# Kernel tuning notes

Measured on AMD Instinct MI355X. Metric: run time of the kernel, lower is better.

Reference implementation:

```python
import jax, jax.numpy as jnp
import numpy as np

N_NODES = 10000
N_EDGES = 160000
HID = 256
NBOND = 6
NATOM = 62
NLAYERS = 6


def _lin_init(key, fan_in, fan_out):
    # torch nn.Linear default: U(-1/sqrt(fan_in), 1/sqrt(fan_in))
    kw, kb = jax.random.split(key)
    bound = 1.0 / np.sqrt(fan_in)
    w = jax.random.uniform(kw, (fan_in, fan_out), jnp.float32, -bound, bound)
    b = jax.random.uniform(kb, (fan_out,), jnp.float32, -bound, bound)
    return w, b


def setup_inputs() -> dict:
    key = jax.random.key(0)
    ks = jax.random.split(key, 32)
    atom_features = jax.random.normal(ks[0], (N_NODES, NATOM), jnp.float32)
    edge_index = jax.random.randint(ks[1], (2, N_EDGES), 0, N_NODES, jnp.int64 if jax.config.jax_enable_x64 else jnp.int32)
    edge_features = jax.random.normal(ks[2], (N_EDGES, NBOND), jnp.float32)

    embed_w, embed_b = _lin_init(ks[3], NATOM, HID)

    msg_in = 2 * HID + NBOND  # 518
    mw1, mb1, mw2, mb2 = [], [], [], []
    uw1, ub1, uw2, ub2 = [], [], [], []
    for i in range(NLAYERS):
        k = jax.random.split(ks[4 + i], 4)
        w, b = _lin_init(k[0], msg_in, HID); mw1.append(w); mb1.append(b)
        w, b = _lin_init(k[1], HID, HID); mw2.append(w); mb2.append(b)
        w, b = _lin_init(k[2], 2 * HID, HID); uw1.append(w); ub1.append(b)
        w, b = _lin_init(k[3], HID, HID); uw2.append(w); ub2.append(b)

    r_w1, r_b1 = _lin_init(ks[20], HID, HID)
    r_w2, r_b2 = _lin_init(ks[21], HID, HID // 2)
    r_w3, r_b3 = _lin_init(ks[22], HID // 2, 1)

    return {
        "atom_features": atom_features,
        "edge_index": edge_index,
        "edge_features": edge_features,
        "embed_w": embed_w, "embed_b": embed_b,
        "msg_w1": jnp.stack(mw1), "msg_b1": jnp.stack(mb1),
        "msg_w2": jnp.stack(mw2), "msg_b2": jnp.stack(mb2),
        "upd_w1": jnp.stack(uw1), "upd_b1": jnp.stack(ub1),
        "upd_w2": jnp.stack(uw2), "upd_b2": jnp.stack(ub2),
        "r_w1": r_w1, "r_b1": r_b1,
        "r_w2": r_w2, "r_b2": r_b2,
        "r_w3": r_w3, "r_b3": r_b3,
    }


def _mlp2(x, w1, b1, w2, b2):
    return jnp.maximum(x @ w1 + b1, 0.0) @ w2 + b2


def reference(atom_features, edge_index, edge_features,
              embed_w, embed_b,
              msg_w1, msg_b1, msg_w2, msg_b2,
              upd_w1, upd_b1, upd_w2, upd_b2,
              r_w1, r_b1, r_w2, r_b2, r_w3, r_b3):
    src, dst = edge_index[0], edge_index[1]
    n = atom_features.shape[0]
    x = atom_features @ embed_w + embed_b  # [N, H]
    for l in range(msg_w1.shape[0]):
        # per-edge gather + concat -> message MLP
        msg_in = jnp.concatenate([x[src], x[dst], edge_features], axis=-1)  # [E, 2H+B]
        msgs = _mlp2(msg_in, msg_w1[l], msg_b1[l], msg_w2[l], msg_b2[l])  # [E, H]
        # scatter-add into dst nodes
        agg = jax.ops.segment_sum(msgs, dst, num_segments=n)  # [N, H]
        x = _mlp2(jnp.concatenate([x, agg], axis=-1), upd_w1[l], upd_b1[l], upd_w2[l], upd_b2[l])
    # readout (dropout is identity in eval mode)
    h = jnp.maximum(x @ r_w1 + r_b1, 0.0)
    h = jnp.maximum(h @ r_w2 + r_b2, 0.0)
    out = h @ r_w3 + r_b3  # [N, 1]
    return out.mean(axis=0)  # [1]
```

## Files before the change

kernel.cpp:

```cpp
#include <hip/hip_runtime.h>
#include <hip/hip_bf16.h>
#include <hip/hip_fp16.h>


#define HID 256

typedef _Float16 h8 __attribute__((ext_vector_type(8)));
typedef float f32x4 __attribute__((ext_vector_type(4)));

__device__ __forceinline__ void unpack_h8(const int4& r, float* f) {
    const __half2* h = reinterpret_cast<const __half2*>(&r);
#pragma unroll
    for (int k = 0; k < 4; ++k) {
        float2 t = __half22float2(h[k]);
        f[2 * k] = t.x;
        f[2 * k + 1] = t.y;
    }
}

__device__ __forceinline__ void unpack_h4(const int2& r, float* f) {
    const __half2* h = reinterpret_cast<const __half2*>(&r);
    float2 t0 = __half22float2(h[0]);
    float2 t1 = __half22float2(h[1]);
    f[0] = t0.x; f[1] = t0.y; f[2] = t1.x; f[3] = t1.y;
}

__device__ __forceinline__ void gld16(const void* g, void* l) {
    __builtin_amdgcn_global_load_lds(
        (const __attribute__((address_space(1))) void*)g,
        (__attribute__((address_space(3))) void*)l, 16, 0, 0);
}

__device__ __forceinline__ int swz(int row) { return (row + (row >> 2)) & 3; }


struct CDesc {
    const float* src;
    __half* dst;
    int Kreal, Kpad, srcN, tile0, dstStride;
};
struct CTab {
    CDesc d[32];
    int nd;
};

__device__ void convert_body(const CTab& tab, int bid) {
    int idx = 0;
    for (int i = 1; i < tab.nd; ++i)
        if (tab.d[i].tile0 <= bid) idx = i;
    const CDesc d = tab.d[idx];
    const int q = bid - d.tile0;
    const int ntN = d.srcN >> 6;
    const int kb = (q / ntN) * 32;
    const int nb = (q % ntN) * 64;
    const int n = nb + (threadIdx.x & 63);
    const int k0 = kb + (threadIdx.x >> 6) * 8;
    h8 v;
#pragma unroll
    for (int j = 0; j < 8; ++j) {
        int k = k0 + j;
        v[j] = (_Float16)((k < d.Kreal) ? d.src[(size_t)k * d.srcN + n] : 0.f);
    }
    *reinterpret_cast<h8*>(&d.dst[(size_t)n * d.dstStride + k0]) = v;
}


__global__ void hist_conv_kernel(const int* __restrict__ dst, int* __restrict__ deg,
                                 int E, const float* __restrict__ atom,
                                 __half* __restrict__ atomH, int NA,
                                 int histB, CTab tab) {
    if ((int)blockIdx.x < histB) {
        int i = blockIdx.x * blockDim.x + threadIdx.x;
        if (i < E) atomicAdd(&deg[dst[i]], 1);
        if (i < NA) {
            int r = i >> 3, seg = i & 7;
            h8 v;
#pragma unroll
            for (int j = 0; j < 8; ++j) {
                int c = seg * 8 + j;
                v[j] = (_Float16)((c < 62) ? atom[(size_t)r * 62 + c] : 0.f);
            }
            *reinterpret_cast<h8*>(&atomH[(size_t)r * 64 + seg * 8]) = v;
        }
    } else {
        convert_body(tab, blockIdx.x - histB);
    }
}

__global__ __launch_bounds__(256) void scan_kernel(
    const int* __restrict__ deg, int* __restrict__ offs, float* __restrict__ degf, int n) {
    __shared__ int ws[4];
    const int t = threadIdx.x;
    const int lane = t & 63;
    const int w = t >> 6;
    const int per = (n + 255) / 256;
    const int s = t * per;
    const int e = min(s + per, n);
    int sum = 0;
    for (int i = s; i < e; ++i) sum += deg[i];
    int v = sum;
#pragma unroll
    for (int off = 1; off < 64; off <<= 1) {
        int u = __shfl_up(v, off, 64);
        if (lane >= off) v += u;
    }
    if (lane == 63) ws[w] = v;
    __syncthreads();
    if (t == 0) {
        int c = 0;
#pragma unroll
        for (int i = 0; i < 4; ++i) { int x = ws[i]; ws[i] = c; c += x; }
    }
    __syncthreads();
    int run = ws[w] + v - sum;
    for (int i = s; i < e; ++i) {
        int d = deg[i];
        offs[i] = run;
        degf[i] = (float)d;
        run += d;
    }
    if (e == n) offs[n] = run;
}


struct BDesc { float* out; const float* base; const float* v1; const float* B1;
               const float* v2; const float* B2; };
struct BTab { BDesc d[31]; };


#define ASTR 40

struct FDesc { const float* U2; const __half* Wfb; __half* dst; int stride; };
struct FTab { FDesc d[22]; };

__device__ void fold_tile(unsigned char* ldsraw, const FDesc& dd, int t4) {
    _Float16* Ah = (_Float16*)ldsraw;
    _Float16* Bh = (_Float16*)(ldsraw + 64 * ASTR * 2);
    const int rowBase = (t4 >> 2) * 64;
    const int colBase = (t4 & 3) * 64;

    const int tid = threadIdx.x;
    const int lane = tid & 63;
    const int wave = tid >> 6;
    const int waveM = (wave >> 1) * 32;
    const int waveN = (wave & 1) * 32;
    const int m0 = lane & 15;
    const int quad = lane >> 4;
    const int sr = tid >> 2;
    const int sseg = tid & 3;

    const f32x4 z = {0.f, 0.f, 0.f, 0.f};
    f32x4 acc[2][2] = {{z, z}, {z, z}};

    for (int kb = 0; kb < 256; kb += 32) {
        {
            size_t off = (size_t)(rowBase + sr) * 256 + kb + sseg * 8;
            *reinterpret_cast<int4*>(&Ah[sr * ASTR + sseg * 8]) =
                *reinterpret_cast<const int4*>(&dd.Wfb[off]);
        }
        {
            const float* Bp = dd.U2 + (size_t)(colBase + sr) * 256 + kb + sseg * 8;
            float4 u0 = *reinterpret_cast<const float4*>(Bp);
            float4 u1 = *reinterpret_cast<const float4*>(Bp + 4);
            h8 v;
            v[0] = (_Float16)u0.x; v[1] = (_Float16)u0.y;
            v[2] = (_Float16)u0.z; v[3] = (_Float16)u0.w;
            v[4] = (_Float16)u1.x; v[5] = (_Float16)u1.y;
            v[6] = (_Float16)u1.z; v[7] = (_Float16)u1.w;
            *reinterpret_cast<h8*>(&Bh[sr * ASTR + sseg * 8]) = v;
        }
        __syncthreads();

        const h8 a0 = *reinterpret_cast<const h8*>(&Ah[(waveM + m0) * ASTR + quad * 8]);
        const h8 a1 = *reinterpret_cast<const h8*>(&Ah[(waveM + 16 + m0) * ASTR + quad * 8]);
        const h8 b0 = *reinterpret_cast<const h8*>(&Bh[(waveN + m0) * ASTR + quad * 8]);
        const h8 b1 = *reinterpret_cast<const h8*>(&Bh[(waveN + 16 + m0) * ASTR + quad * 8]);

        acc[0][0] = __builtin_amdgcn_mfma_f32_16x16x32_f16(a0, b0, acc[0][0], 0, 0, 0);
        acc[0][1] = __builtin_amdgcn_mfma_f32_16x16x32_f16(a0, b1, acc[0][1], 0, 0, 0);
        acc[1][0] = __builtin_amdgcn_mfma_f32_16x16x32_f16(a1, b0, acc[1][0], 0, 0, 0);
        acc[1][1] = __builtin_amdgcn_mfma_f32_16x16x32_f16(a1, b1, acc[1][1], 0, 0, 0);

        __syncthreads();
    }

#pragma unroll
    for (int tm = 0; tm < 2; ++tm)
#pragma unroll
        for (int reg = 0; reg < 4; ++reg) {
            int n = rowBase + waveM + tm * 16 + quad * 4 + reg;
#pragma unroll
            for (int tn = 0; tn < 2; ++tn) {
                int k = colBase + waveN + tn * 16 + m0;
                dd.dst[(size_t)n * dd.stride + k] = __float2half_rn(acc[tm][tn][reg]);
            }
        }
}


template <int TN>
__device__ void gemm_tile(
    unsigned char* lds, int bx, int by,
    const __half* __restrict__ A, int lda,
    const __half* __restrict__ W, int K,
    const float* __restrict__ bias,
    __half* __restrict__ C, int M, int Nc, int do_relu) {
    constexpr int BUF = 4096 + TN * 2048;

    const int tid = threadIdx.x;
    const int lane = tid & 63;
    const int wave = tid >> 6;
    const int m0 = lane & 15;
    const int quad = lane >> 4;
    const int waveM = (wave >> 1) * 32;
    const int waveN = (wave & 1) * (TN * 16);
    const int rowBase = bx * 64;
    const int colBase = by * (TN * 32);

    const int sa_r = tid >> 2;
    const int sa_ks = (tid & 3) ^ swz(sa_r);
    const int sa_row = min(rowBase + sa_r, M - 1);
    const int sb_r1 = sa_r + 64;
    const int sb_ks1 = (tid & 3) ^ swz(sb_r1);

    int aoff[2], boff[TN];
#pragma unroll
    for (int tm = 0; tm < 2; ++tm) {
        int r = waveM + tm * 16 + m0;
        aoff[tm] = ((r << 2) + (quad ^ swz(r))) << 4;
    }
#pragma unroll
    for (int tn = 0; tn < TN; ++tn) {
        int r = waveN + tn * 16 + m0;
        boff[tn] = 4096 + (((r << 2) + (quad ^ swz(r))) << 4);
    }

    const f32x4 z = {0.f, 0.f, 0.f, 0.f};
    f32x4 acc[2][TN];
#pragma unroll
    for (int tm = 0; tm < 2; ++tm)
#pragma unroll
        for (int tn = 0; tn < TN; ++tn) acc[tm][tn] = z;

    const __half* ga = A + (size_t)sa_row * lda + sa_ks * 8;
    const __half* gb0 = W + (size_t)(colBase + sa_r) * K + sa_ks * 8;
    const __half* gb1 = W + (size_t)(colBase + sb_r1) * K + sb_ks1 * 8;

    auto issue = [&](int p, int kb) {
        unsigned char* base = lds + p * BUF;
        gld16(ga + kb, base + wave * 1024);
        gld16(gb0 + kb, base + 4096 + wave * 1024);
        if constexpr (TN == 4) gld16(gb1 + kb, base + 8192 + wave * 1024);
    };

    issue(0, 0);
    int p = 0;
    for (int kb = 0; kb < K; kb += 32) {
        const bool has_next = (kb + 32 < K);
        if (has_next) issue(p ^ 1, kb + 32);
        if (has_next) {
            if constexpr (TN == 4)
                asm volatile("s_waitcnt vmcnt(3)" ::: "memory");
            else
                asm volatile("s_waitcnt vmcnt(2)" ::: "memory");
        } else {
            asm volatile("s_waitcnt vmcnt(0)" ::: "memory");
        }
        asm volatile("s_barrier" ::: "memory");

        const unsigned char* base = lds + p * BUF;
        h8 ah[2], bh[TN];
#pragma unroll
        for (int tm = 0; tm < 2; ++tm)
            ah[tm] = *reinterpret_cast<const h8*>(base + aoff[tm]);
#pragma unroll
        for (int tn = 0; tn < TN; ++tn)
            bh[tn] = *reinterpret_cast<const h8*>(base + boff[tn]);
#pragma unroll
        for (int tm = 0; tm < 2; ++tm)
#pragma unroll
            for (int tn = 0; tn < TN; ++tn)
                acc[tm][tn] = __builtin_amdgcn_mfma_f32_16x16x32_f16(
                    ah[tm], bh[tn], acc[tm][tn], 0, 0, 0);
        asm volatile("s_waitcnt lgkmcnt(0)" ::: "memory");
        asm volatile("s_barrier" ::: "memory");
        p ^= 1;
    }

    float cb[TN];
    int col[TN];
#pragma unroll
    for (int tn = 0; tn < TN; ++tn) {
        col[tn] = colBase + waveN + tn * 16 + m0;
        cb[tn] = bias ? bias[col[tn]] : 0.f;
    }
#pragma unroll
    for (int tm = 0; tm < 2; ++tm) {
#pragma unroll
        for (int reg = 0; reg < 4; ++reg) {
            int row = rowBase + waveM + tm * 16 + quad * 4 + reg;
            if (row >= M) continue;
#pragma unroll
            for (int tn = 0; tn < TN; ++tn) {
                float v = acc[tm][tn][reg] + cb[tn];
                if (do_relu) v = fmaxf(v, 0.f);
                C[(size_t)row * Nc + col[tn]] = __float2half_rn(v);
            }
        }
    }
}


__global__ __launch_bounds__(256) void scatter_fold_bias_embed_kernel(
    const int* __restrict__ src, const int* __restrict__ dst,
    const int* __restrict__ offs, int* __restrict__ cursor,
    int* __restrict__ csr_src, const float* __restrict__ ef,
    __half* __restrict__ ef8, int E, int sblocks,
    FTab ft, BTab bt, int fblocks, int bblocks,
    const __half* __restrict__ atomH, const __half* __restrict__ w_emb,
    const float* __restrict__ emb_b, __half* __restrict__ outX,
    int M, int mblk64) {
    __shared__ __align__(16) unsigned char lds[16384];
    int b = blockIdx.x;
    if (b < sblocks) {
        int i = b * 256 + (int)threadIdx.x;
        if (i < E) {
            int d = dst[i];
            int pos = atomicAdd(&cursor[d], 1);
            int idx = offs[d] + pos;
            csr_src[idx] = src[i];
            const float* s6 = ef + (size_t)i * 6;
            unsigned short h[8];
#pragma unroll
            for (int j = 0; j < 6; ++j) h[j] = __half_as_ushort(__float2half_rn(s6[j]));
            h[6] = 0; h[7] = 0;
            int4 pk;
            pk.x = (int)(h[0] | ((unsigned)h[1] << 16));
            pk.y = (int)(h[2] | ((unsigned)h[3] << 16));
            pk.z = (int)(h[4] | ((unsigned)h[5] << 16));
            pk.w = (int)(h[6] | ((unsigned)h[7] << 16));
            *reinterpret_cast<int4*>(ef8 + (size_t)idx * 8) = pk;
        }
        return;
    }
    b -= sblocks;
    if (b < fblocks) {
        fold_tile(lds, ft.d[b >> 4], b & 15);
        return;
    }
    b -= fblocks;
    if (b < bblocks) {
        const BDesc d = bt.d[b];
        const int j = threadIdx.x;
        float acc = d.base ? d.base[j] : 0.f;
        if (d.v1)
            for (int k = 0; k < 256; ++k) acc = fmaf(d.v1[k], d.B1[(size_t)k * 256 + j], acc);
        if (d.v2)
            for (int k = 0; k < 256; ++k) acc = fmaf(d.v2[k], d.B2[(size_t)k * 256 + j], acc);
        d.out[j] = acc;
        return;
    }
    b -= bblocks;
    gemm_tile<2>(lds, b % mblk64, b / mblk64, atomH, 64, w_emb, 64,
                 emb_b, outX, M, HID, 0);
}


__global__ __launch_bounds__(256) void gemm128(
    const __half* __restrict__ A, int lda, const __half* __restrict__ A2,
    const __half* __restrict__ W, int K,
    const float* __restrict__ bias, const float* __restrict__ bias2,
    const float* __restrict__ rowscale,
    __half* __restrict__ C, int M, int Nc, int do_relu) {
    __shared__ __align__(16) unsigned char lds[2 * 16384];

    const int tid = threadIdx.x;
    const int lane = tid & 63;
    const int wave = tid >> 6;
    const int m0 = lane & 15;
    const int quad = lane >> 4;
    const int waveM = (wave >> 1) * 64;
    const int waveN = (wave & 1) * 64;
    const int rowBase = (int)blockIdx.x * 128;
    const int colBase = (int)blockIdx.y * 128;

    const __half* ga[2];
    const __half* ga2[2];
    const __half* gb[2];
    int adst[2], bdst[2];
#pragma unroll
    for (int j = 0; j < 2; ++j) {
        int seg = j * 256 + wave * 64 + lane;
        int r = seg >> 2;
        int ks = (seg & 3) ^ swz(r);
        int arow = min(rowBase + r, M - 1);
        ga[j] = A + (size_t)arow * lda + ks * 8;
        ga2[j] = A2 ? A2 + (size_t)arow * lda + ks * 8 : nullptr;
        gb[j] = W + (size_t)(colBase + r) * K + ks * 8;
        adst[j] = (j * 4 + wave) * 1024;
        bdst[j] = 8192 + (j * 4 + wave) * 1024;
    }

    int aoff[4], boff[4];
#pragma unroll
    for (int i = 0; i < 4; ++i) {
        int r = waveM + i * 16 + m0;
        aoff[i] = ((r << 2) + (quad ^ swz(r))) << 4;
        int rb = waveN + i * 16 + m0;
        boff[i] = 8192 + (((rb << 2) + (quad ^ swz(rb))) << 4);
    }

    const f32x4 z = {0.f, 0.f, 0.f, 0.f};
    f32x4 acc[4][4];
#pragma unroll
    for (int i = 0; i < 4; ++i)
#pragma unroll
        for (int j = 0; j < 4; ++j) acc[i][j] = z;

    auto issue = [&](int p, int kb) {
        unsigned char* base = lds + p * 16384;
        const bool hi = (A2 != nullptr) && (kb >= 256);
        const int ko = hi ? (kb - 256) : kb;
#pragma unroll
        for (int j = 0; j < 2; ++j)
            gld16((hi ? ga2[j] : ga[j]) + ko, base + adst[j]);
#pragma unroll
        for (int j = 0; j < 2; ++j)
            gld16(gb[j] + kb, base + bdst[j]);
    };

    issue(0, 0);
    int p = 0;
    for (int kb = 0; kb < K; kb += 32) {
        const bool has_next = (kb + 32 < K);
        if (has_next) issue(p ^ 1, kb + 32);
        if (has_next) asm volatile("s_waitcnt vmcnt(4)" ::: "memory");
        else          asm volatile("s_waitcnt vmcnt(0)" ::: "memory");
        asm volatile("s_barrier" ::: "memory");

        const unsigned char* base = lds + p * 16384;
        h8 ah[4], bh[4];
#pragma unroll
        for (int i = 0; i < 4; ++i) ah[i] = *reinterpret_cast<const h8*>(base + aoff[i]);
#pragma unroll
        for (int j = 0; j < 4; ++j) bh[j] = *reinterpret_cast<const h8*>(base + boff[j]);
#pragma unroll
        for (int i = 0; i < 4; ++i)
#pragma unroll
            for (int j = 0; j < 4; ++j)
                acc[i][j] = __builtin_amdgcn_mfma_f32_16x16x32_f16(
                    ah[i], bh[j], acc[i][j], 0, 0, 0);
        asm volatile("s_waitcnt lgkmcnt(0)" ::: "memory");
        asm volatile("s_barrier" ::: "memory");
        p ^= 1;
    }

    float cb[4], db[4];
    int col[4];
#pragma unroll
    for (int j = 0; j < 4; ++j) {
        col[j] = colBase + waveN + j * 16 + m0;
        cb[j] = bias ? bias[col[j]] : 0.f;
        db[j] = bias2 ? bias2[col[j]] : 0.f;
    }
#pragma unroll
    for (int i = 0; i < 4; ++i) {
#pragma unroll
        for (int reg = 0; reg < 4; ++reg) {
            int row = rowBase + waveM + i * 16 + quad * 4 + reg;
            if (row >= M) continue;
            float rs = rowscale ? rowscale[row] : 0.0f;
#pragma unroll
            for (int j = 0; j < 4; ++j) {
                float v = acc[i][j][reg] + cb[j] + rs * db[j];
                if (do_relu) v = fmaxf(v, 0.f);
                C[(size_t)row * Nc + col[j]] = __float2half_rn(v);
            }
        }
    }
}


__global__ __launch_bounds__(256) void aggregate_kernel(
    const __half* __restrict__ PQ, const __half* __restrict__ ef8,
    const int* __restrict__ offs, const int* __restrict__ csr_src,
    const float* __restrict__ W1c, __half* __restrict__ Hagg, int n) {
    const int wave = threadIdx.x >> 6;
    const int lane = threadIdx.x & 63;
    const int node = blockIdx.x * 4 + wave;
    if (node >= n) return;
    const int ch = lane * 4;

    float wc[6][4];
#pragma unroll
    for (int k = 0; k < 6; ++k) {
        float4 w0 = *reinterpret_cast<const float4*>(W1c + k * HID + ch);
        wc[k][0] = w0.x; wc[k][1] = w0.y; wc[k][2] = w0.z; wc[k][3] = w0.w;
    }
    float qb[4];
    unpack_h4(*reinterpret_cast<const int2*>(PQ + (size_t)node * 512 + 256 + ch), qb);

    float acc[4] = {0.f, 0.f, 0.f, 0.f};

    auto fma_edge = [&](const int2& praw, const int4& eraw) {
        float p[4], e[8];
        unpack_h4(praw, p);
        unpack_h8(eraw, e);
#pragma unroll
        for (int i = 0; i < 4; ++i) {
            float h = p[i] + qb[i];
            h = fmaf(e[0], wc[0][i], h);
            h = fmaf(e[1], wc[1][i], h);
            h = fmaf(e[2], wc[2][i], h);
            h = fmaf(e[3], wc[3][i], h);
            h = fmaf(e[4], wc[4][i], h);
            h = fmaf(e[5], wc[5][i], h);
            acc[i] += fmaxf(h, 0.f);
        }
    };

    const int beg = offs[node];
    const int end = offs[node + 1];
    int j = beg;

    while (j + 6 <= end) {
        int s0 = csr_src[j];
        int s1 = csr_src[j + 1];
        int s2 = csr_src[j + 2];
        int s3 = csr_src[j + 3];
        int s4 = csr_src[j + 4];
        int s5 = csr_src[j + 5];
        int4 e0 = *reinterpret_cast<const int4*>(ef8 + (size_t)j * 8);
        int4 e1 = *reinterpret_cast<const int4*>(ef8 + (size_t)(j + 1) * 8);
        int4 e2 = *reinterpret_cast<const int4*>(ef8 + (size_t)(j + 2) * 8);
        int4 e3 = *reinterpret_cast<const int4*>(ef8 + (size_t)(j + 3) * 8);
        int4 e4 = *reinterpret_cast<const int4*>(ef8 + (size_t)(j + 4) * 8);
        int4 e5 = *reinterpret_cast<const int4*>(ef8 + (size_t)(j + 5) * 8);
        int2 p0 = *reinterpret_cast<const int2*>(PQ + (size_t)s0 * 512 + ch);
        int2 p1 = *reinterpret_cast<const int2*>(PQ + (size_t)s1 * 512 + ch);
        int2 p2 = *reinterpret_cast<const int2*>(PQ + (size_t)s2 * 512 + ch);
        int2 p3 = *reinterpret_cast<const int2*>(PQ + (size_t)s3 * 512 + ch);
        int2 p4 = *reinterpret_cast<const int2*>(PQ + (size_t)s4 * 512 + ch);
        int2 p5 = *reinterpret_cast<const int2*>(PQ + (size_t)s5 * 512 + ch);
        fma_edge(p0, e0);
        fma_edge(p1, e1);
        fma_edge(p2, e2);
        fma_edge(p3, e3);
        fma_edge(p4, e4);
        fma_edge(p5, e5);
        j += 6;
    }
    while (j + 2 <= end) {
        int s0 = csr_src[j];
        int s1 = csr_src[j + 1];
        int4 e0 = *reinterpret_cast<const int4*>(ef8 + (size_t)j * 8);
        int4 e1 = *reinterpret_cast<const int4*>(ef8 + (size_t)(j + 1) * 8);
        int2 p0 = *reinterpret_cast<const int2*>(PQ + (size_t)s0 * 512 + ch);
        int2 p1 = *reinterpret_cast<const int2*>(PQ + (size_t)s1 * 512 + ch);
        fma_edge(p0, e0);
        fma_edge(p1, e1);
        j += 2;
    }
    if (j < end) {
        int s = csr_src[j];
        int4 e = *reinterpret_cast<const int4*>(ef8 + (size_t)j * 8);
        int2 pw = *reinterpret_cast<const int2*>(PQ + (size_t)s * 512 + ch);
        fma_edge(pw, e);
    }

    unsigned short hs[4];
#pragma unroll
    for (int i = 0; i < 4; ++i) hs[i] = __half_as_ushort(__float2half_rn(acc[i]));
    int2 pk;
    pk.x = (int)(hs[0] | ((unsigned)hs[1] << 16));
    pk.y = (int)(hs[2] | ((unsigned)hs[3] << 16));
    *reinterpret_cast<int2*>(Hagg + (size_t)node * HID + ch) = pk;
}


__global__ __launch_bounds__(256) void readout_kernel(
    const __half* __restrict__ U5, const __half* __restrict__ wF,
    const float* __restrict__ cbF, const __half* __restrict__ wR2,
    const float* __restrict__ bR2, const float* __restrict__ w3,
    const float* __restrict__ b3, float* __restrict__ accum,
    int* __restrict__ done, float* __restrict__ outp, int M, int nblocks) {
    __shared__ __align__(16) unsigned char lds[24576 + 64 * 272 * 2];
    _Float16* h1 = (_Float16*)(lds + 24576);

    const int tid = threadIdx.x;
    const int lane = tid & 63;
    const int wave = tid >> 6;
    const int m0 = lane & 15;
    const int quad = lane >> 4;
    const int waveM = (wave >> 1) * 32;
    const int waveN = (wave & 1) * 64;
    const int rowBase = blockIdx.x * 64;

    const int sa_r = tid >> 2;
    const int sa_ks = (tid & 3) ^ swz(sa_r);
    const int sa_row = min(rowBase + sa_r, M - 1);
    const int sb_r1 = sa_r + 64;
    const int sb_ks1 = (tid & 3) ^ swz(sb_r1);

    int aoff[2], boff[4];
#pragma unroll
    for (int tm = 0; tm < 2; ++tm) {
        int r = waveM + tm * 16 + m0;
        aoff[tm] = ((r << 2) + (quad ^ swz(r))) << 4;
    }
#pragma unroll
    for (int tn = 0; tn < 4; ++tn) {
        int r = waveN + tn * 16 + m0;
        boff[tn] = (((r << 2) + (quad ^ swz(r))) << 4);
    }

    constexpr int BUF = 4096 + 4 * 2048;
    const f32x4 z = {0.f, 0.f, 0.f, 0.f};

    for (int half = 0; half < 2; ++half) {
        const __half* W = wF + (size_t)(half * 128) * 256;
        f32x4 acc[2][4] = {{z, z, z, z}, {z, z, z, z}};
        const __half* ga = U5 + (size_t)sa_row * 256 + sa_ks * 8;
        const __half* gb0 = W + (size_t)sa_r * 256 + sa_ks * 8;
        const __half* gb1 = W + (size_t)sb_r1 * 256 + sb_ks1 * 8;

        auto issue = [&](int p, int kb) {
            unsigned char* base = lds + p * BUF;
            gld16(ga + kb, base + wave * 1024);
            gld16(gb0 + kb, base + 4096 + wave * 1024);
            gld16(gb1 + kb, base + 8192 + wave * 1024);
        };
        issue(0, 0);
        int p = 0;
        for (int kb = 0; kb < 256; kb += 32) {
            const bool has_next = (kb + 32 < 256);
            if (has_next) issue(p ^ 1, kb + 32);
            if (has_next) asm volatile("s_waitcnt vmcnt(3)" ::: "memory");
            else asm volatile("s_waitcnt vmcnt(0)" ::: "memory");
            asm volatile("s_barrier" ::: "memory");
            const unsigned char* base = lds + p * BUF;
            h8 ah[2], bh[4];
#pragma unroll
            for (int tm = 0; tm < 2; ++tm)
                ah[tm] = *reinterpret_cast<const h8*>(base + aoff[tm]);
#pragma unroll
            for (int tn = 0; tn < 4; ++tn)
                bh[tn] = *reinterpret_cast<const h8*>(base + 4096 + boff[tn]);
#pragma unroll
            for (int tm = 0; tm < 2; ++tm)
#pragma unroll
                for (int tn = 0; tn < 4; ++tn)
                    acc[tm][tn] = __builtin_amdgcn_mfma_f32_16x16x32_f16(
                        ah[tm], bh[tn], acc[tm][tn], 0, 0, 0);
            asm volatile("s_waitcnt lgkmcnt(0)" ::: "memory");
            asm volatile("s_barrier" ::: "memory");
            p ^= 1;
        }
#pragma unroll
        for (int tm = 0; tm < 2; ++tm)
#pragma unroll
            for (int reg = 0; reg < 4; ++reg) {
                int r = waveM + tm * 16 + quad * 4 + reg;
#pragma unroll
                for (int tn = 0; tn < 4; ++tn) {
                    int c = half * 128 + waveN + tn * 16 + m0;
                    float v = acc[tm][tn][reg] + cbF[c];
                    h1[r * 272 + c] = (_Float16)fmaxf(v, 0.f);
                }
            }
        __syncthreads();
    }

    f32x4 acc2[2][4] = {{z, z, z, z}, {z, z, z, z}};
    auto issueB = [&](int p, int kb) {
        unsigned char* base = lds + p * 8192;
        gld16(wR2 + (size_t)sa_r * 256 + sa_ks * 8 + kb, base + wave * 1024);
        gld16(wR2 + (size_t)sb_r1 * 256 + sb_ks1 * 8 + kb, base + 4096 + wave * 1024);
    };
    issueB(0, 0);
    int p = 0;
    for (int kb = 0; kb < 256; kb += 32) {
        const bool has_next = (kb + 32 < 256);
        if (has_next) issueB(p ^ 1, kb + 32);
        if (has_next) asm volatile("s_waitcnt vmcnt(2)" ::: "memory");
        else asm volatile("s_waitcnt vmcnt(0)" ::: "memory");
        asm volatile("s_barrier" ::: "memory");
        const unsigned char* base = lds + p * 8192;
        h8 ah[2], bh[4];
#pragma unroll
        for (int tm = 0; tm < 2; ++tm)
            ah[tm] = *reinterpret_cast<const h8*>(
                &h1[(waveM + tm * 16 + m0) * 272 + kb + quad * 8]);
#pragma unroll
        for (int tn = 0; tn < 4; ++tn)
            bh[tn] = *reinterpret_cast<const h8*>(base + boff[tn]);
#pragma unroll
        for (int tm = 0; tm < 2; ++tm)
#pragma unroll
            for (int tn = 0; tn < 4; ++tn)
                acc2[tm][tn] = __builtin_amdgcn_mfma_f32_16x16x32_f16(
                    ah[tm], bh[tn], acc2[tm][tn], 0, 0, 0);
        asm volatile("s_waitcnt lgkmcnt(0)" ::: "memory");
        asm volatile("s_barrier" ::: "memory");
        p ^= 1;
    }

    float s = 0.f;
#pragma unroll
    for (int tm = 0; tm < 2; ++tm)
#pragma unroll
        for (int reg = 0; reg < 4; ++reg) {
            int row = rowBase + waveM + tm * 16 + quad * 4 + reg;
            if (row >= M) continue;
#pragma unroll
            for (int tn = 0; tn < 4; ++tn) {
                int c = waveN + tn * 16 + m0;
                float v = acc2[tm][tn][reg] + bR2[c];
                s += fmaxf(v, 0.f) * w3[c];
            }
        }
    __syncthreads();
    float* red = (float*)lds;
    red[tid] = s;
    __syncthreads();
    for (int off = 128; off > 0; off >>= 1) {
        if (tid < off) red[tid] += red[tid + off];
        __syncthreads();
    }
    if (tid == 0) {
        atomicAdd(accum, red[0]);
        __threadfence();
        int old = atomicAdd(done, 1);
        if (old == nblocks - 1) {
            float tot = atomicAdd(accum, 0.0f);
            outp[0] = tot / (float)M + b3[0];
        }
    }
}


extern "C" void kernel_launch(void* const* d_in, const int* in_sizes, int n_in,
                              void* d_out, int out_size, void* d_ws, size_t ws_size,
                              hipStream_t stream) {
    const float* atom   = (const float*)d_in[0];
    const int*   eidx   = (const int*)d_in[1];
    const float* ef     = (const float*)d_in[2];
    const float* emb_w  = (const float*)d_in[3];
    const float* emb_b  = (const float*)d_in[4];
    const float* msg_w1 = (const float*)d_in[5];
    const float* msg_b1 = (const float*)d_in[6];
    const float* msg_w2 = (const float*)d_in[7];
    const float* msg_b2 = (const float*)d_in[8];
    const float* upd_w1 = (const float*)d_in[9];
    const float* upd_b1 = (const float*)d_in[10];
    const float* upd_w2 = (const float*)d_in[11];
    const float* upd_b2 = (const float*)d_in[12];
    const float* r_w1   = (const float*)d_in[13];
    const float* r_b1   = (const float*)d_in[14];
    const float* r_w2   = (const float*)d_in[15];
    const float* r_b2   = (const float*)d_in[16];
    const float* r_w3   = (const float*)d_in[17];
    const float* r_b3   = (const float*)d_in[18];

    const int N = in_sizes[0] / 62;
    const int E = in_sizes[1] / 2;
    const int L = in_sizes[5] / (518 * 256);
    const int* src = eidx;
    const int* dst = eidx + E;

    char* wp = (char*)d_ws;
    auto alloc = [&](size_t bytes) -> void* {
        void* p = (void*)wp;
        wp += (bytes + 255) & ~(size_t)255;
        return p;
    };
    int*   deg     = (int*)alloc((size_t)N * 4);
    int*   cursor  = (int*)alloc((size_t)N * 4);
    float* accum   = (float*)alloc(256);
    int*   done    = (int*)((char*)accum + 16);
    size_t zero_bytes = (size_t)((char*)accum - (char*)d_ws) + 256;
    float* degf    = (float*)alloc((size_t)N * 4);
    int*   offs    = (int*)alloc((size_t)(N + 1) * 4);
    int*   csr_src = (int*)alloc((size_t)E * 4);
    __half* ef8    = (__half*)alloc((size_t)E * 8 * 2);

    const int SQ_P = 256 * 256;
    __half* w_emb = (__half*)alloc((size_t)256 * 64 * 2);
    __half* w_r2  = (__half*)alloc((size_t)128 * 256 * 2);
    __half* wF    = (__half*)alloc((size_t)SQ_P * 2);
    __half *wPQ[6], *wUPD[6];
    for (int l = 0; l < L; ++l) {
        wPQ[l]  = (__half*)alloc((size_t)512 * 256 * 2);
        wUPD[l] = (__half*)alloc((size_t)256 * 512 * 2);
    }
    __half* fb[22];
    for (int i = 0; i < 22; ++i) fb[i] = (__half*)alloc((size_t)SQ_P * 2);
    float* bvec = (float*)alloc((size_t)19 * 256 * 4);
    float* b512 = (float*)alloc((size_t)L * 512 * 4);

    __half* atomH = (__half*)alloc((size_t)N * 64 * 2);
    __half* bufX0 = (__half*)alloc((size_t)N * HID * 2);
    __half* bufX1 = (__half*)alloc((size_t)N * HID * 2);
    __half* PQ    = (__half*)alloc((size_t)N * 512 * 2);
    __half* HaggH = (__half*)alloc((size_t)N * HID * 2);

    hipMemsetAsync(d_ws, 0, zero_bytes, stream);

    CTab ct1;
    int nd = 0, tiles = 0;
    auto addDesc = [&](const float* s, __half* dh, int Kreal, int Kpad, int srcN,
                       int dstStride) {
        ct1.d[nd] = {s, dh, Kreal, Kpad, srcN, tiles, dstStride};
        tiles += (Kpad / 32) * (srcN / 64);
        ++nd;
    };
    addDesc(emb_w, w_emb, 62, 64, 256, 64);
    addDesc(msg_w1, wPQ[0], 256, 256, 256, 256);
    addDesc(msg_w1 + 256 * 256, wPQ[0] + SQ_P, 256, 256, 256, 256);
    addDesc(upd_w1, wUPD[0] + 256, 256, 256, 256, 512);
    addDesc(r_w2, w_r2, 256, 256, 128, 256);
    for (int l = 1; l < L; ++l) {
        addDesc(msg_w1 + (size_t)l * 518 * 256,             fb[l - 1], 256, 256, 256, 256);
        addDesc(msg_w1 + (size_t)l * 518 * 256 + 256 * 256, fb[4 + l], 256, 256, 256, 256);
        addDesc(upd_w1 + (size_t)l * 512 * 256,             fb[9 + l], 256, 256, 256, 256);
    }
    for (int l = 0; l < L; ++l)
        addDesc(upd_w1 + (size_t)l * 512 * 256 + 256 * 256, fb[15 + l], 256, 256, 256, 256);
    addDesc(r_w1, fb[21], 256, 256, 256, 256);
    ct1.nd = nd;

    const int hag = max(E, N * 8);
    const int histB = (hag + 255) / 256;
    hist_conv_kernel<<<histB + tiles, 256, 0, stream>>>(
        dst, deg, E, atom, atomH, N * 8, histB, ct1);

    scan_kernel<<<1, 256, 0, stream>>>(deg, offs, degf, N);

    FTab ft;
    for (int l = 1; l < L; ++l) {
        const float* U2p = upd_w2 + (size_t)(l - 1) * SQ_P;
        ft.d[l - 1] = {U2p, fb[l - 1], wPQ[l], 256};
        ft.d[4 + l] = {U2p, fb[4 + l], wPQ[l] + SQ_P, 256};
        ft.d[9 + l] = {U2p, fb[9 + l], wUPD[l] + 256, 512};
    }
    for (int l = 0; l < L; ++l)
        ft.d[15 + l] = {msg_w2 + (size_t)l * SQ_P, fb[15 + l], wUPD[l], 512};
    ft.d[21] = {upd_w2 + (size_t)5 * SQ_P, fb[21], wF, 256};

    BTab bt;
    int nb = 0;
    for (int l = 0; l < L; ++l) {
        const float* ub2p = (l > 0) ? upd_b2 + (size_t)(l - 1) * 256 : nullptr;
        bt.d[nb++] = {b512 + (size_t)l * 512 + 256, msg_b1 + (size_t)l * 256,
                      ub2p, msg_w1 + (size_t)l * 518 * 256,
                      ub2p, msg_w1 + (size_t)l * 518 * 256 + 256 * 256};
        bt.d[nb++] = {b512 + (size_t)l * 512, nullptr, nullptr, nullptr, nullptr, nullptr};
        bt.d[nb++] = {bvec + (size_t)(6 + l) * 256, upd_b1 + (size_t)l * 256,
                      ub2p, upd_w1 + (size_t)l * 512 * 256, nullptr, nullptr};
        bt.d[nb++] = {bvec + (size_t)(12 + l) * 256, nullptr,
                      msg_b2 + (size_t)l * 256, upd_w1 + (size_t)l * 512 * 256 + 256 * 256,
                      nullptr, nullptr};
    }
    bt.d[nb++] = {bvec + (size_t)18 * 256, r_b1, upd_b2 + (size_t)5 * 256, r_w1,
                  nullptr, nullptr};

    const int sblocks = (E + 255) / 256;
    const int fblocks = 22 * 16;
    const int mblk64 = (N + 63) / 64;
    scatter_fold_bias_embed_kernel<<<sblocks + fblocks + nb + mblk64 * 4, 256, 0,
                                     stream>>>(
        src, dst, offs, cursor, csr_src, ef, ef8, E, sblocks,
        ft, bt, fblocks, nb, atomH, w_emb, emb_b, bufX0, N, mblk64);

    const int mblkR = (N + 127) / 128;
    __half* U_prev = bufX0;
    __half* U_next = bufX1;
    for (int l = 0; l < L; ++l) {
        const float* w1c = msg_w1 + (size_t)l * 518 * 256 + 512 * 256;

        gemm128<<<dim3(mblkR, 4), 256, 0, stream>>>(
            U_prev, HID, nullptr, wPQ[l], HID,
            b512 + (size_t)l * 512, nullptr, nullptr,
            PQ, N, 512, 0);
        aggregate_kernel<<<(N + 3) / 4, 256, 0, stream>>>(
            PQ, ef8, offs, csr_src, w1c, HaggH, N);
        gemm128<<<dim3(mblkR, 2), 256, 0, stream>>>(
            HaggH, HID, U_prev, wUPD[l], 512,
            bvec + (size_t)(6 + l) * 256, bvec + (size_t)(12 + l) * 256, degf,
            U_next, N, 256, 1);
        __half* t = U_prev; U_prev = U_next; U_next = t;
    }

    readout_kernel<<<mblk64, 256, 0, stream>>>(
        U_prev, wF, bvec + (size_t)18 * 256, w_r2, r_b2, r_w3, r_b3,
        accum, done, (float*)d_out, N, mblk64);
}
```

Measured before the change: 464.5 us.

## Shrink GEMM tiles to 64-row blocks and fold scan into histogram kernel

Replaces the 128x128-tile GEMM with a templated 64-row tile (64x128 for the PQ projection, 64x64 for the update), so each layer launches many more blocks to fill the CUs at N=10000. The single-block scan kernel is merged into the histogram/convert kernel using a last-block-done atomic counter, which removes one launch. Smaller tiles reduce per-block data reuse and add more redundant weight loads. The last-block pattern depends on the counter being zeroed every call.

New measurement: 591.1 us. +27.3%, slower.

```diff
diff --git a/kernel.cpp b/kernel.cpp
--- a/kernel.cpp
+++ b/kernel.cpp
@@ -65,10 +65,13 @@
 }
 
 
-__global__ void hist_conv_kernel(const int* __restrict__ dst, int* __restrict__ deg,
-                                 int E, const float* __restrict__ atom,
-                                 __half* __restrict__ atomH, int NA,
-                                 int histB, CTab tab) {
+__global__ void hist_conv_scan_kernel(
+    const int* __restrict__ dst, int* __restrict__ deg, int E,
+    const float* __restrict__ atom, __half* __restrict__ atomH, int NA,
+    int histB, CTab tab, int* __restrict__ k1done,
+    int* __restrict__ offs, float* __restrict__ degf, int n) {
+    __shared__ int ws[4];
+    __shared__ int lastFlag;
     if ((int)blockIdx.x < histB) {
         int i = blockIdx.x * blockDim.x + threadIdx.x;
         if (i < E) atomicAdd(&deg[dst[i]], 1);
@@ -85,11 +88,17 @@
     } else {
         convert_body(tab, blockIdx.x - histB);
     }
-}
-
-__global__ __launch_bounds__(256) void scan_kernel(
-    const int* __restrict__ deg, int* __restrict__ offs, float* __restrict__ degf, int n) {
-    __shared__ int ws[4];
+
+    __threadfence();
+    __syncthreads();
+    if (threadIdx.x == 0) {
+        int old = atomicAdd(k1done, 1);
+        lastFlag = (old == (int)gridDim.x - 1);
+    }
+    __syncthreads();
+    if (!lastFlag) return;
+    __threadfence();
+
     const int t = threadIdx.x;
     const int lane = t & 63;
     const int w = t >> 6;
@@ -366,67 +375,62 @@
 }
 
 
-__global__ __launch_bounds__(256) void gemm128(
+template <int TN>
+__global__ __launch_bounds__(256) void mfma_gemm(
     const __half* __restrict__ A, int lda, const __half* __restrict__ A2,
     const __half* __restrict__ W, int K,
     const float* __restrict__ bias, const float* __restrict__ bias2,
     const float* __restrict__ rowscale,
     __half* __restrict__ C, int M, int Nc, int do_relu) {
-    __shared__ __align__(16) unsigned char lds[2 * 16384];
+    constexpr int BUF = 4096 + TN * 2048;
+    __shared__ __align__(16) unsigned char lds[2 * BUF];
 
     const int tid = threadIdx.x;
     const int lane = tid & 63;
     const int wave = tid >> 6;
     const int m0 = lane & 15;
     const int quad = lane >> 4;
-    const int waveM = (wave >> 1) * 64;
-    const int waveN = (wave & 1) * 64;
-    const int rowBase = (int)blockIdx.x * 128;
-    const int colBase = (int)blockIdx.y * 128;
-
-    const __half* ga[2];
-    const __half* ga2[2];
-    const __half* gb[2];
-    int adst[2], bdst[2];
-#pragma unroll
-    for (int j = 0; j < 2; ++j) {
-        int seg = j * 256 + wave * 64 + lane;
-        int r = seg >> 2;
-        int ks = (seg & 3) ^ swz(r);
-        int arow = min(rowBase + r, M - 1);
-        ga[j] = A + (size_t)arow * lda + ks * 8;
-        ga2[j] = A2 ? A2 + (size_t)arow * lda + ks * 8 : nullptr;
-        gb[j] = W + (size_t)(colBase + r) * K + ks * 8;
-        adst[j] = (j * 4 + wave) * 1024;
-        bdst[j] = 8192 + (j * 4 + wave) * 1024;
-    }
-
-    int aoff[4], boff[4];
-#pragma unroll
-    for (int i = 0; i < 4; ++i) {
-        int r = waveM + i * 16 + m0;
-        aoff[i] = ((r << 2) + (quad ^ swz(r))) << 4;
-        int rb = waveN + i * 16 + m0;
-        boff[i] = 8192 + (((rb << 2) + (quad ^ swz(rb))) << 4);
+    const int waveM = (wave >> 1) * 32;
+    const int waveN = (wave & 1) * (TN * 16);
+    const int rowBase = blockIdx.x * 64;
+    const int colBase = blockIdx.y * (TN * 32);
+
+    const int sa_r = tid >> 2;
+    const int sa_ks = (tid & 3) ^ swz(sa_r);
+    const int sa_row = min(rowBase + sa_r, M - 1);
+    const int sb_r1 = sa_r + 64;
+    const int sb_ks1 = (tid & 3) ^ swz(sb_r1);
+
+    int aoff[2], boff[TN];
+#pragma unroll
+    for (int tm = 0; tm < 2; ++tm) {
+        int r = waveM + tm * 16 + m0;
+        aoff[tm] = ((r << 2) + (quad ^ swz(r))) << 4;
+    }
+#pragma unroll
+    for (int tn = 0; tn < TN; ++tn) {
+        int r = waveN + tn * 16 + m0;
+        boff[tn] = 4096 + (((r << 2) + (quad ^ swz(r))) << 4);
     }
 
     const f32x4 z = {0.f, 0.f, 0.f, 0.f};
-    f32x4 acc[4][4];
-#pragma unroll
-    for (int i = 0; i < 4; ++i)
-#pragma unroll
-        for (int j = 0; j < 4; ++j) acc[i][j] = z;
+    f32x4 acc[2][TN];
+#pragma unroll
+    for (int tm = 0; tm < 2; ++tm)
+#pragma unroll
+        for (int tn = 0; tn < TN; ++tn) acc[tm][tn] = z;
+
+    const __half* ga = A + (size_t)sa_row * lda + sa_ks * 8;
+    const __half* ga2 = A2 ? A2 + (size_t)sa_row * lda + sa_ks * 8 : nullptr;
+    const __half* gb0 = W + (size_t)(colBase + sa_r) * K + sa_ks * 8;
+    const __half* gb1 = W + (size_t)(colBase + sb_r1) * K + sb_ks1 * 8;
 
     auto issue = [&](int p, int kb) {
-        unsigned char* base = lds + p * 16384;
-        const bool hi = (A2 != nullptr) && (kb >= 256);
-        const int ko = hi ? (kb - 256) : kb;
-#pragma unroll
-        for (int j = 0; j < 2; ++j)
-            gld16((hi ? ga2[j] : ga[j]) + ko, base + adst[j]);
-#pragma unroll
-        for (int j = 0; j < 2; ++j)
-            gld16(gb[j] + kb, base + bdst[j]);
+        unsigned char* base = lds + p * BUF;
+        const __half* as = (A2 && kb >= 256) ? (ga2 + (kb - 256)) : (ga + kb);
+        gld16(as, base + wave * 1024);
+        gld16(gb0 + kb, base + 4096 + wave * 1024);
+        if constexpr (TN == 4) gld16(gb1 + kb, base + 8192 + wave * 1024);
     };
 
     issue(0, 0);
@@ -434,47 +438,55 @@
     for (int kb = 0; kb < K; kb += 32) {
         const bool has_next = (kb + 32 < K);
         if (has_next) issue(p ^ 1, kb + 32);
-        if (has_next) asm volatile("s_waitcnt vmcnt(4)" ::: "memory");
-        else          asm volatile("s_waitcnt vmcnt(0)" ::: "memory");
+        if (has_next) {
+            if constexpr (TN == 4)
+                asm volatile("s_waitcnt vmcnt(3)" ::: "memory");
+            else
+                asm volatile("s_waitcnt vmcnt(2)" ::: "memory");
+        } else {
+            asm volatile("s_waitcnt vmcnt(0)" ::: "memory");
+        }
         asm volatile("s_barrier" ::: "memory");
 
-        const unsigned char* base = lds + p * 16384;
-        h8 ah[4], bh[4];
-#pragma unroll
-        for (int i = 0; i < 4; ++i) ah[i] = *reinterpret_cast<const h8*>(base + aoff[i]);
-#pragma unroll
-        for (int j = 0; j < 4; ++j) bh[j] = *reinterpret_cast<const h8*>(base + boff[j]);
-#pragma unroll
-        for (int i = 0; i < 4; ++i)
-#pragma unroll
-            for (int j = 0; j < 4; ++j)
-                acc[i][j] = __builtin_amdgcn_mfma_f32_16x16x32_f16(
-                    ah[i], bh[j], acc[i][j], 0, 0, 0);
+        const unsigned char* base = lds + p * BUF;
+        h8 ah[2], bh[TN];
+#pragma unroll
+        for (int tm = 0; tm < 2; ++tm)
+            ah[tm] = *reinterpret_cast<const h8*>(base + aoff[tm]);
+#pragma unroll
+        for (int tn = 0; tn < TN; ++tn)
+            bh[tn] = *reinterpret_cast<const h8*>(base + boff[tn]);
+#pragma unroll
+        for (int tm = 0; tm < 2; ++tm)
+#pragma unroll
+            for (int tn = 0; tn < TN; ++tn)
+                acc[tm][tn] = __builtin_amdgcn_mfma_f32_16x16x32_f16(
+                    ah[tm], bh[tn], acc[tm][tn], 0, 0, 0);
         asm volatile("s_waitcnt lgkmcnt(0)" ::: "memory");
         asm volatile("s_barrier" ::: "memory");
         p ^= 1;
     }
 
-    float cb[4], db[4];
-    int col[4];
-#pragma unroll
-    for (int j = 0; j < 4; ++j) {
-        col[j] = colBase + waveN + j * 16 + m0;
-        cb[j] = bias ? bias[col[j]] : 0.f;
-        db[j] = bias2 ? bias2[col[j]] : 0.f;
-    }
-#pragma unroll
-    for (int i = 0; i < 4; ++i) {
+    float cb[TN], db[TN];
+    int col[TN];
+#pragma unroll
+    for (int tn = 0; tn < TN; ++tn) {
+        col[tn] = colBase + waveN + tn * 16 + m0;
+        cb[tn] = bias ? bias[col[tn]] : 0.f;
+        db[tn] = bias2 ? bias2[col[tn]] : 0.f;
+    }
+#pragma unroll
+    for (int tm = 0; tm < 2; ++tm) {
 #pragma unroll
         for (int reg = 0; reg < 4; ++reg) {
-            int row = rowBase + waveM + i * 16 + quad * 4 + reg;
+            int row = rowBase + waveM + tm * 16 + quad * 4 + reg;
             if (row >= M) continue;
             float rs = rowscale ? rowscale[row] : 0.0f;
 #pragma unroll
-            for (int j = 0; j < 4; ++j) {
-                float v = acc[i][j][reg] + cb[j] + rs * db[j];
+            for (int tn = 0; tn < TN; ++tn) {
+                float v = acc[tm][tn][reg] + cb[tn] + rs * db[tn];
                 if (do_relu) v = fmaxf(v, 0.f);
-                C[(size_t)row * Nc + col[j]] = __float2half_rn(v);
+                C[(size_t)row * Nc + col[tn]] = __float2half_rn(v);
             }
         }
     }
@@ -778,6 +790,7 @@
     int*   cursor  = (int*)alloc((size_t)N * 4);
     float* accum   = (float*)alloc(256);
     int*   done    = (int*)((char*)accum + 16);
+    int*   k1done  = (int*)((char*)accum + 32);
     size_t zero_bytes = (size_t)((char*)accum - (char*)d_ws) + 256;
     float* degf    = (float*)alloc((size_t)N * 4);
     int*   offs    = (int*)alloc((size_t)(N + 1) * 4);
@@ -831,10 +844,8 @@
 
     const int hag = max(E, N * 8);
     const int histB = (hag + 255) / 256;
-    hist_conv_kernel<<<histB + tiles, 256, 0, stream>>>(
-        dst, deg, E, atom, atomH, N * 8, histB, ct1);
-
-    scan_kernel<<<1, 256, 0, stream>>>(deg, offs, degf, N);
+    hist_conv_scan_kernel<<<histB + tiles, 256, 0, stream>>>(
+        dst, deg, E, atom, atomH, N * 8, histB, ct1, k1done, offs, degf, N);
 
     FTab ft;
     for (int l = 1; l < L; ++l) {
@@ -872,26 +883,26 @@
         src, dst, offs, cursor, csr_src, ef, ef8, E, sblocks,
         ft, bt, fblocks, nb, atomH, w_emb, emb_b, bufX0, N, mblk64);
 
-    const int mblkR = (N + 127) / 128;
+    dim3 blk(256);
     __half* U_prev = bufX0;
     __half* U_next = bufX1;
     for (int l = 0; l < L; ++l) {
         const float* w1c = msg_w1 + (size_t)l * 518 * 256 + 512 * 256;
 
-        gemm128<<<dim3(mblkR, 4), 256, 0, stream>>>(
+        mfma_gemm<4><<<dim3(mblk64, 4), blk, 0, stream>>>(
             U_prev, HID, nullptr, wPQ[l], HID,
             b512 + (size_t)l * 512, nullptr, nullptr,
             PQ, N, 512, 0);
-        aggregate_kernel<<<(N + 3) / 4, 256, 0, stream>>>(
+        aggregate_kernel<<<(N + 3) / 4, blk, 0, stream>>>(
             PQ, ef8, offs, csr_src, w1c, HaggH, N);
-        gemm128<<<dim3(mblkR, 2), 256, 0, stream>>>(
+        mfma_gemm<2><<<dim3(mblk64, 4), blk, 0, stream>>>(
             HaggH, HID, U_prev, wUPD[l], 512,
             bvec + (size_t)(6 + l) * 256, bvec + (size_t)(12 + l) * 256, degf,
             U_next, N, 256, 1);
         __half* t = U_prev; U_prev = U_next; U_next = t;
     }
 
-    readout_kernel<<<mblk64, 256, 0, stream>>>(
+    readout_kernel<<<mblk64, blk, 0, stream>>>(
         U_prev, wF, bvec + (size_t)18 * 256, w_r2, r_b2, r_w3, r_b3,
         accum, done, (float*)d_out, N, mblk64);
 }
```
